# Optimization experiments

Hardware: AMD Instinct MI355X
Metric: run time of the kernel (lower is better)

The kernel has to match this reference:

```python
import jax, jax.numpy as jnp
import numpy as np

N_NODES = 100000
N_EDGES = 1600000
VOCAB = 128
D = 30
N_CLASSES = 5


def setup_inputs() -> dict:
    key = jax.random.key(0)
    ks = jax.random.split(key, 8)
    x = jax.random.randint(ks[0], (N_NODES,), 0, VOCAB)
    edge_index = jax.random.randint(ks[1], (2, N_EDGES), 0, N_NODES)
    emb = jax.random.normal(ks[2], (VOCAB, D), dtype=jnp.float32)
    W1 = jax.random.normal(ks[3], (D, D), dtype=jnp.float32) * (1.0 / np.sqrt(D))
    W2 = jax.random.normal(ks[4], (D, D), dtype=jnp.float32) * (1.0 / np.sqrt(D))
    W3 = jax.random.normal(ks[5], (D, D), dtype=jnp.float32) * (1.0 / np.sqrt(D))
    Wout = jax.random.normal(ks[6], (N_CLASSES, D), dtype=jnp.float32) * (1.0 / np.sqrt(D))
    b1 = jnp.zeros((D,), jnp.float32)
    b2 = jnp.zeros((D,), jnp.float32)
    b3 = jnp.zeros((D,), jnp.float32)
    bout = jnp.zeros((N_CLASSES,), jnp.float32)
    return dict(x=x, edge_index=edge_index, emb=emb, W1=W1, b1=b1, W2=W2, b2=b2,
                W3=W3, b3=b3, Wout=Wout, bout=bout)


def _gnn_layer(h, row, col, W, b):
    # h: [N, D]; row/col: [E+N] (self loops appended)
    n = h.shape[0]
    deg = jax.ops.segment_sum(jnp.ones(row.shape, h.dtype), row, num_segments=n)  # [N]
    msg = h[row] / deg[row][:, None]                 # gather + normalize: [E+N, D]
    agg = jax.ops.segment_sum(msg, col, num_segments=n)  # scatter-add: [N, D]
    return jax.nn.relu(agg @ W.T + b)


def reference(x, edge_index, emb, W1, b1, W2, b2, W3, b3, Wout, bout):
    n = x.shape[0]
    loops = jnp.arange(n, dtype=edge_index.dtype)
    row = jnp.concatenate([edge_index[0], loops])  # add_self_loops
    col = jnp.concatenate([edge_index[1], loops])
    h = emb[x]  # [N, D]
    for W, b in ((W1, b1), (W2, b2), (W3, b3)):
        h = _gnn_layer(h, row, col, W, b)
    return h @ Wout.T + bout  # [N, 5]
```

## Files before the change

kernel.cpp:

```cpp
#include <hip/hip_runtime.h>
#include <hip/hip_fp16.h>

#define D 30
#define DP 32
#define NCLS 5
#define VOCAB 128
#define BS 256
#define BSS 512
#define BSHIFT 8
#define BNODES 256
#define NSBMAX 512
#define CAP 8192
#define NBLK_S 256
#define CHUNK 6272
#define LDSCAP 6144
#define NPB 64


__global__ void k_prep(int* __restrict__ gcur, int* __restrict__ rcur, int nsb,
                       const float* __restrict__ emb, float* __restrict__ embp) {
    int i = blockIdx.x * blockDim.x + threadIdx.x;
    if (i < nsb) { gcur[i] = i * CAP; rcur[i] = i * CAP; }
    if (i < VOCAB * DP) {
        int v = i >> 5, c = i & (DP - 1);
        embp[i] = (c < D) ? emb[v * D + c] : 0.0f;
    }
}

__global__ void __launch_bounds__(BSS)
k_scatter3(const int* __restrict__ row, const int* __restrict__ col,
           int* __restrict__ gcur, int* __restrict__ rcur,
           int* __restrict__ ebuf, unsigned char* __restrict__ rbuf,
           int e, int nsb) {
    __shared__ int pay[CHUNK];
    __shared__ unsigned short bof[CHUNK];
    __shared__ int lhist[NSBMAX];
    __shared__ int lscan[NSBMAX];
    __shared__ int lcur[NSBMAX];
    __shared__ int gdst[NSBMAX];
    unsigned char* pay8 = (unsigned char*)pay;

    int phase = blockIdx.x >= NBLK_S;
    int blk = blockIdx.x - phase * NBLK_S;
    const int* key = phase ? row : col;
    int per = (e + NBLK_S - 1) / NBLK_S;
    int s = blk * per; if (s > e) s = e;
    int t = s + per; if (t > e) t = e;
    int m = t - s;
    int tid = threadIdx.x;

    lhist[tid] = 0;
    __syncthreads();
    for (int i = s + tid; i < t; i += BSS)
        atomicAdd(&lhist[key[i] >> BSHIFT], 1);
    __syncthreads();
    lscan[tid] = lhist[tid];
    __syncthreads();
    for (int st = 1; st < NSBMAX; st <<= 1) {
        int tv = (tid >= st) ? lscan[tid - st] : 0;
        __syncthreads();
        lscan[tid] += tv;
        __syncthreads();
    }
    lcur[tid] = lscan[tid] - lhist[tid];
    __syncthreads();
    if (phase == 0) {
        for (int i = s + tid; i < t; i += BSS) {
            int c = col[i], b = c >> BSHIFT;
            int p = atomicAdd(&lcur[b], 1);
            pay[p] = (row[i] << BSHIFT) | (c & (BNODES - 1));
            bof[p] = (unsigned short)b;
        }
    } else {
        for (int i = s + tid; i < t; i += BSS) {
            int r = row[i], b = r >> BSHIFT;
            int p = atomicAdd(&lcur[b], 1);
            pay8[p] = (unsigned char)(r & (BNODES - 1));
            bof[p] = (unsigned short)b;
        }
    }
    __syncthreads();
    int* cur = phase ? rcur : gcur;
    if (tid < nsb) {
        int h = lhist[tid];
        gdst[tid] = h ? atomicAdd(&cur[tid], h) : 0;
    }
    __syncthreads();
    if (phase == 0) {
        for (int p = tid; p < m; p += BSS) {
            int b = bof[p];
            ebuf[gdst[b] + (p - (lscan[b] - lhist[b]))] = pay[p];
        }
    } else {
        for (int p = tid; p < m; p += BSS) {
            int b = bof[p];
            rbuf[gdst[b] + (p - (lscan[b] - lhist[b]))] = pay8[p];
        }
    }
}

__global__ void __launch_bounds__(BS)
k_odbsort(int* __restrict__ ebuf, const unsigned char* __restrict__ rbuf,
          const int* __restrict__ gcur, const int* __restrict__ rcur,
          const int* __restrict__ x, float* __restrict__ rdeg, int2* __restrict__ xr,
          int* __restrict__ off, int* __restrict__ cnt, int n, int nsb) {
    __shared__ int ledge[LDSCAP];
    __shared__ int c256[BNODES];
    __shared__ int b256[BNODES];
    __shared__ int cur256[BNODES];
    int side = blockIdx.x >= nsb;
    int bkt = side ? blockIdx.x - nsb : blockIdx.x;
    int tid = threadIdx.x;
    int base = bkt * CAP;

    if (side == 0) {
        int rm = rcur[bkt] - base;
        c256[tid] = 0;
        __syncthreads();
        for (int k = tid; k < rm; k += BS)
            atomicAdd(&c256[rbuf[base + k]], 1);
        __syncthreads();
        int node = (bkt << BSHIFT) + tid;
        if (node < n) {
            float rd = 1.0f / (float)(c256[tid] + 1);
            rdeg[node] = rd;
            xr[node] = make_int2(x[node], __float_as_int(rd));
        }
    } else {
        int m = gcur[bkt] - base;
        if (m > LDSCAP) m = LDSCAP;
        for (int k = tid; k < m; k += BS) ledge[k] = ebuf[base + k];
        c256[tid] = 0;
        __syncthreads();
        for (int k = tid; k < m; k += BS)
            atomicAdd(&c256[ledge[k] & (BNODES - 1)], 1);
        __syncthreads();
        b256[tid] = c256[tid];
        __syncthreads();
        for (int st = 1; st < BNODES; st <<= 1) {
            int tv = (tid >= st) ? b256[tid - st] : 0;
            __syncthreads();
            b256[tid] += tv;
            __syncthreads();
        }
        cur256[tid] = b256[tid] - c256[tid];
        int node = (bkt << BSHIFT) + tid;
        if (node < n) {
            off[node] = base + b256[tid] - c256[tid];
            cnt[node] = c256[tid];
        }
        __syncthreads();
        for (int k = tid; k < m; k += BS) {
            int v = ledge[k];
            int p = atomicAdd(&cur256[v & (BNODES - 1)], 1);
            ebuf[base + p] = v >> BSHIFT;
        }
    }
}

__device__ __forceinline__ void acc8h(float4 raw, float* acc) {
    const __half2* h = (const __half2*)&raw;
#pragma unroll
    for (int u = 0; u < 4; ++u) {
        float2 f = __half22float2(h[u]);
        acc[2 * u] += f.x; acc[2 * u + 1] += f.y;
    }
}
__device__ __forceinline__ void fma4(float4 a, float4 w, float& d) {
    d = fmaf(a.x, w.x, d); d = fmaf(a.y, w.y, d);
    d = fmaf(a.z, w.z, d); d = fmaf(a.w, w.w, d);
}

__global__ void __launch_bounds__(BS)
k_agg_lin(const __half* __restrict__ Ain, const int2* __restrict__ xr,
          const float* __restrict__ embp,
          const int* __restrict__ off, const int* __restrict__ cnt,
          const int* __restrict__ esrc, const float* __restrict__ rdeg,
          const float* __restrict__ W, const float* __restrict__ bias,
          const float* __restrict__ Wout, const float* __restrict__ bout,
          __half* __restrict__ Aout, float* __restrict__ out,
          int n, int srcmode, int outmode) {
    __shared__ float aggS[NPB * DP];
    __shared__ float WsP[DP * DP];
    __shared__ float bsP[DP];
    __shared__ float h3S[NPB * DP];
    __shared__ float WoP[NCLS * DP];
    __shared__ float boS[NCLS];
    const float4* Ain4  = (const float4*)Ain;
    const float4* embp4 = (const float4*)embp;
    int tid = threadIdx.x;
    int i0 = blockIdx.x * NPB;
    int j = tid >> 2;
    int q = tid & 3;
    int i = i0 + j;
    for (int p = tid; p < DP * DP; p += BS) {
        int rr = p >> 5, ccx = p & 31;
        WsP[p] = (rr < D && ccx < D) ? W[rr * D + ccx] : 0.0f;
    }
    if (tid < DP) bsP[tid] = (tid < D) ? bias[tid] : 0.0f;
    if (outmode == 1) {
        for (int p = tid; p < NCLS * DP; p += BS) {
            int rr = p >> 5, ccx = p & 31;
            WoP[p] = (ccx < D) ? Wout[rr * D + ccx] : 0.0f;
        }
        if (tid < NCLS) boS[tid] = bout[tid];
    }
    float acc[8];
#pragma unroll
    for (int u = 0; u < 8; ++u) acc[u] = 0.0f;
    if (i < n) {
        int base = off[i], c = cnt[i], k = 0;
        if (srcmode == 0) {
            acc8h(Ain4[(size_t)i * 4 + q], acc);
            for (; k + 16 <= c; k += 16) {
                float4 av[16];
#pragma unroll
                for (int u = 0; u < 16; ++u)
                    av[u] = Ain4[(size_t)esrc[base + k + u] * 4 + q];
#pragma unroll
                for (int u = 0; u < 16; ++u) acc8h(av[u], acc);
            }
            for (; k + 4 <= c; k += 4) {
                float4 av[4];
#pragma unroll
                for (int u = 0; u < 4; ++u)
                    av[u] = Ain4[(size_t)esrc[base + k + u] * 4 + q];
#pragma unroll
                for (int u = 0; u < 4; ++u) acc8h(av[u], acc);
            }
            for (; k < c; ++k)
                acc8h(Ain4[(size_t)esrc[base + k] * 4 + q], acc);
        } else {
            int2 xi = xr[i];
            float ri = __int_as_float(xi.y);
            float4 e0 = embp4[(size_t)xi.x * 8 + 2 * q];
            float4 e1 = embp4[(size_t)xi.x * 8 + 2 * q + 1];
            acc[0] = e0.x * ri; acc[1] = e0.y * ri; acc[2] = e0.z * ri; acc[3] = e0.w * ri;
            acc[4] = e1.x * ri; acc[5] = e1.y * ri; acc[6] = e1.z * ri; acc[7] = e1.w * ri;
            for (; k + 4 <= c; k += 4) {
                int2 xv[4];
#pragma unroll
                for (int u = 0; u < 4; ++u) xv[u] = xr[esrc[base + k + u]];
#pragma unroll
                for (int u = 0; u < 4; ++u) {
                    float rr = __int_as_float(xv[u].y);
                    float4 f0 = embp4[(size_t)xv[u].x * 8 + 2 * q];
                    float4 f1 = embp4[(size_t)xv[u].x * 8 + 2 * q + 1];
                    acc[0] = fmaf(f0.x, rr, acc[0]); acc[1] = fmaf(f0.y, rr, acc[1]);
                    acc[2] = fmaf(f0.z, rr, acc[2]); acc[3] = fmaf(f0.w, rr, acc[3]);
                    acc[4] = fmaf(f1.x, rr, acc[4]); acc[5] = fmaf(f1.y, rr, acc[5]);
                    acc[6] = fmaf(f1.z, rr, acc[6]); acc[7] = fmaf(f1.w, rr, acc[7]);
                }
            }
            for (; k < c; ++k) {
                int2 xs = xr[esrc[base + k]];
                float rr = __int_as_float(xs.y);
                float4 f0 = embp4[(size_t)xs.x * 8 + 2 * q];
                float4 f1 = embp4[(size_t)xs.x * 8 + 2 * q + 1];
                acc[0] = fmaf(f0.x, rr, acc[0]); acc[1] = fmaf(f0.y, rr, acc[1]);
                acc[2] = fmaf(f0.z, rr, acc[2]); acc[3] = fmaf(f0.w, rr, acc[3]);
                acc[4] = fmaf(f1.x, rr, acc[4]); acc[5] = fmaf(f1.y, rr, acc[5]);
                acc[6] = fmaf(f1.z, rr, acc[6]); acc[7] = fmaf(f1.w, rr, acc[7]);
            }
        }
    }
    ((float4*)aggS)[j * 8 + 2 * q]     = make_float4(acc[0], acc[1], acc[2], acc[3]);
    ((float4*)aggS)[j * 8 + 2 * q + 1] = make_float4(acc[4], acc[5], acc[6], acc[7]);
    __syncthreads();

    {
        int cc = tid & 31;
        int jg = tid >> 5;
        const float4* wrow = (const float4*)&WsP[cc * DP];
        float4 w0 = wrow[0], w1 = wrow[1], w2 = wrow[2], w3 = wrow[3];
        float4 w4 = wrow[4], w5 = wrow[5], w6 = wrow[6], w7 = wrow[7];
        float bb = bsP[cc];
        if (outmode == 0) {
            for (int jj = jg; jj < NPB; jj += 8) {
                int nd = i0 + jj;
                if (nd >= n) break;
                const float4* ar = (const float4*)&aggS[jj * DP];
                float a = bb;
                fma4(ar[0], w0, a); fma4(ar[1], w1, a); fma4(ar[2], w2, a); fma4(ar[3], w3, a);
                fma4(ar[4], w4, a); fma4(ar[5], w5, a); fma4(ar[6], w6, a); fma4(ar[7], w7, a);
                a = fmaxf(a, 0.0f) * rdeg[nd];
                if (cc >= D) a = 0.0f;
                Aout[(size_t)nd * DP + cc] = __float2half_rn(a);
            }
        } else {
            for (int jj = jg; jj < NPB; jj += 8) {
                const float4* ar = (const float4*)&aggS[jj * DP];
                float a = bb;
                fma4(ar[0], w0, a); fma4(ar[1], w1, a); fma4(ar[2], w2, a); fma4(ar[3], w3, a);
                fma4(ar[4], w4, a); fma4(ar[5], w5, a); fma4(ar[6], w6, a); fma4(ar[7], w7, a);
                h3S[jj * DP + cc] = (cc < D) ? fmaxf(a, 0.0f) : 0.0f;
            }
            __syncthreads();
            for (int it = tid; it < NPB * NCLS; it += BS) {
                int jj = it / NCLS, cc2 = it - jj * NCLS;
                int nd = i0 + jj;
                if (nd >= n) continue;
                const float4* hr = (const float4*)&h3S[jj * DP];
                const float4* wr2 = (const float4*)&WoP[cc2 * DP];
                float a = boS[cc2];
#pragma unroll
                for (int u = 0; u < 8; ++u) fma4(hr[u], wr2[u], a);
                out[(size_t)nd * NCLS + cc2] = a;
            }
        }
    }
}


extern "C" void kernel_launch(void* const* d_in, const int* in_sizes, int n_in,
                              void* d_out, int out_size, void* d_ws, size_t ws_size,
                              hipStream_t stream) {
    const int*   x    = (const int*)d_in[0];
    const int*   ei   = (const int*)d_in[1];
    const float* emb  = (const float*)d_in[2];
    const float* W1   = (const float*)d_in[3];
    const float* b1   = (const float*)d_in[4];
    const float* W2   = (const float*)d_in[5];
    const float* b2   = (const float*)d_in[6];
    const float* W3   = (const float*)d_in[7];
    const float* b3   = (const float*)d_in[8];
    const float* Wout = (const float*)d_in[9];
    const float* bout = (const float*)d_in[10];
    float* out = (float*)d_out;

    const int N = in_sizes[0];
    const int E = in_sizes[1] / 2;
    const int* row = ei;
    const int* col = ei + E;
    const int nsb = (N + BNODES - 1) >> BSHIFT;

    __half* A0  = (__half*)d_ws;
    __half* A1  = A0 + (size_t)N * DP;
    float* embp = (float*)(A1 + (size_t)N * DP);
    float* rdeg = embp + VOCAB * DP;
    int2*  xr   = (int2*)(rdeg + N);
    int*   ebuf = (int*)(xr + N);
    unsigned char* rbuf = (unsigned char*)(ebuf + (size_t)nsb * CAP);
    int*   off  = (int*)(rbuf + (((size_t)nsb * CAP + 3) & ~(size_t)3));
    int*   cnt  = off + N;
    int*   gcur = cnt + N;
    int*   rcur = gcur + nsb;

    dim3 blk(BS);

    k_prep<<<dim3((VOCAB * DP + BS - 1) / BS), blk, 0, stream>>>(gcur, rcur, nsb, emb, embp);
    k_scatter3<<<dim3(2 * NBLK_S), dim3(BSS), 0, stream>>>(row, col, gcur, rcur,
                                                           ebuf, rbuf, E, nsb);
    k_odbsort<<<dim3(2 * nsb), blk, 0, stream>>>(ebuf, rbuf, gcur, rcur, x,
                                                 rdeg, xr, off, cnt, N, nsb);

    dim3 gAgg((N + NPB - 1) / NPB);
    k_agg_lin<<<gAgg, blk, 0, stream>>>(nullptr, xr, embp, off, cnt, ebuf, rdeg,
                                        W1, b1, Wout, bout, A1, out, N, 1, 0);
    k_agg_lin<<<gAgg, blk, 0, stream>>>(A1, xr, embp, off, cnt, ebuf, rdeg,
                                        W2, b2, Wout, bout, A0, out, N, 0, 0);
    k_agg_lin<<<gAgg, blk, 0, stream>>>(A0, xr, embp, off, cnt, ebuf, rdeg,
                                        W3, b3, Wout, bout, A1, out, N, 0, 1);
}
```

Measured before the change: 208.4 us.

## Pad per-node edge lists to multiples of 8 with a zero dummy node

```diff
diff --git a/kernel.cpp b/kernel.cpp
--- a/kernel.cpp
+++ b/kernel.cpp
@@ -13,18 +13,25 @@
 #define CAP 8192
 #define NBLK_S 256
 #define CHUNK 6272
-#define LDSCAP 6144
+#define LDSCAP 8192
 #define NPB 64
 
 
 __global__ void k_prep(int* __restrict__ gcur, int* __restrict__ rcur, int nsb,
-                       const float* __restrict__ emb, float* __restrict__ embp) {
+                       const float* __restrict__ emb, float* __restrict__ embp,
+                       __half* __restrict__ A0, __half* __restrict__ A1,
+                       int2* __restrict__ xr, int n) {
     int i = blockIdx.x * blockDim.x + threadIdx.x;
     if (i < nsb) { gcur[i] = i * CAP; rcur[i] = i * CAP; }
     if (i < VOCAB * DP) {
         int v = i >> 5, c = i & (DP - 1);
         embp[i] = (c < D) ? emb[v * D + c] : 0.0f;
     }
+    if (i < DP) {
+        A0[(size_t)n * DP + i] = __float2half_rn(0.0f);
+        A1[(size_t)n * DP + i] = __float2half_rn(0.0f);
+    }
+    if (i == 0) xr[n] = make_int2(0, 0);
 }
 
 __global__ void __launch_bounds__(BSS)
@@ -106,6 +113,7 @@
           int* __restrict__ off, int* __restrict__ cnt, int n, int nsb) {
     __shared__ int ledge[LDSCAP];
     __shared__ int c256[BNODES];
+    __shared__ int p256[BNODES];
     __shared__ int b256[BNODES];
     __shared__ int cur256[BNODES];
     int side = blockIdx.x >= nsb;
@@ -135,7 +143,9 @@
         for (int k = tid; k < m; k += BS)
             atomicAdd(&c256[ledge[k] & (BNODES - 1)], 1);
         __syncthreads();
-        b256[tid] = c256[tid];
+        int pc = (c256[tid] + 7) & ~7;
+        p256[tid] = pc;
+        b256[tid] = pc;
         __syncthreads();
         for (int st = 1; st < BNODES; st <<= 1) {
             int tv = (tid >= st) ? b256[tid - st] : 0;
@@ -143,18 +153,23 @@
             b256[tid] += tv;
             __syncthreads();
         }
-        cur256[tid] = b256[tid] - c256[tid];
+        int mybase = base + b256[tid] - p256[tid];
+        cur256[tid] = mybase;
         int node = (bkt << BSHIFT) + tid;
         if (node < n) {
-            off[node] = base + b256[tid] - c256[tid];
-            cnt[node] = c256[tid];
+            off[node] = mybase;
+            cnt[node] = p256[tid];
         }
         __syncthreads();
         for (int k = tid; k < m; k += BS) {
             int v = ledge[k];
             int p = atomicAdd(&cur256[v & (BNODES - 1)], 1);
-            ebuf[base + p] = v >> BSHIFT;
-        }
+            ebuf[base + (p - base)] = v >> BSHIFT;
+        }
+        __syncthreads();
+        int realend = cur256[tid];
+        int padend = mybase + p256[tid];
+        for (int p = realend; p < padend; ++p) ebuf[p] = n;
     }
 }
 
@@ -183,7 +198,6 @@
     __shared__ float aggS[NPB * DP];
     __shared__ float WsP[DP * DP];
     __shared__ float bsP[DP];
-    __shared__ float h3S[NPB * DP];
     __shared__ float WoP[NCLS * DP];
     __shared__ float boS[NCLS];
     const float4* Ain4  = (const float4*)Ain;
@@ -209,27 +223,23 @@
 #pragma unroll
     for (int u = 0; u < 8; ++u) acc[u] = 0.0f;
     if (i < n) {
-        int base = off[i], c = cnt[i], k = 0;
+        int base = off[i], c = cnt[i];
         if (srcmode == 0) {
             acc8h(Ain4[(size_t)i * 4 + q], acc);
-            for (; k + 16 <= c; k += 16) {
-                float4 av[16];
-#pragma unroll
-                for (int u = 0; u < 16; ++u)
-                    av[u] = Ain4[(size_t)esrc[base + k + u] * 4 + q];
-#pragma unroll
-                for (int u = 0; u < 16; ++u) acc8h(av[u], acc);
-            }
-            for (; k + 4 <= c; k += 4) {
-                float4 av[4];
-#pragma unroll
-                for (int u = 0; u < 4; ++u)
-                    av[u] = Ain4[(size_t)esrc[base + k + u] * 4 + q];
-#pragma unroll
-                for (int u = 0; u < 4; ++u) acc8h(av[u], acc);
-            }
-            for (; k < c; ++k)
-                acc8h(Ain4[(size_t)esrc[base + k] * 4 + q], acc);
+            for (int k = 0; k < c; k += 8) {
+                int4 ea = *(const int4*)(esrc + base + k);
+                int4 eb = *(const int4*)(esrc + base + k + 4);
+                float4 a0 = Ain4[(size_t)ea.x * 4 + q];
+                float4 a1 = Ain4[(size_t)ea.y * 4 + q];
+                float4 a2 = Ain4[(size_t)ea.z * 4 + q];
+                float4 a3 = Ain4[(size_t)ea.w * 4 + q];
+                float4 a4 = Ain4[(size_t)eb.x * 4 + q];
+                float4 a5 = Ain4[(size_t)eb.y * 4 + q];
+                float4 a6 = Ain4[(size_t)eb.z * 4 + q];
+                float4 a7 = Ain4[(size_t)eb.w * 4 + q];
+                acc8h(a0, acc); acc8h(a1, acc); acc8h(a2, acc); acc8h(a3, acc);
+                acc8h(a4, acc); acc8h(a5, acc); acc8h(a6, acc); acc8h(a7, acc);
+            }
         } else {
             int2 xi = xr[i];
             float ri = __int_as_float(xi.y);
@@ -237,12 +247,14 @@
             float4 e1 = embp4[(size_t)xi.x * 8 + 2 * q + 1];
             acc[0] = e0.x * ri; acc[1] = e0.y * ri; acc[2] = e0.z * ri; acc[3] = e0.w * ri;
             acc[4] = e1.x * ri; acc[5] = e1.y * ri; acc[6] = e1.z * ri; acc[7] = e1.w * ri;
-            for (; k + 4 <= c; k += 4) {
-                int2 xv[4];
-#pragma unroll
-                for (int u = 0; u < 4; ++u) xv[u] = xr[esrc[base + k + u]];
-#pragma unroll
-                for (int u = 0; u < 4; ++u) {
+            for (int k = 0; k < c; k += 8) {
+                int4 ea = *(const int4*)(esrc + base + k);
+                int4 eb = *(const int4*)(esrc + base + k + 4);
+                int2 xv[8];
+                xv[0] = xr[ea.x]; xv[1] = xr[ea.y]; xv[2] = xr[ea.z]; xv[3] = xr[ea.w];
+                xv[4] = xr[eb.x]; xv[5] = xr[eb.y]; xv[6] = xr[eb.z]; xv[7] = xr[eb.w];
+#pragma unroll
+                for (int u = 0; u < 8; ++u) {
                     float rr = __int_as_float(xv[u].y);
                     float4 f0 = embp4[(size_t)xv[u].x * 8 + 2 * q];
                     float4 f1 = embp4[(size_t)xv[u].x * 8 + 2 * q + 1];
@@ -251,16 +263,6 @@
                     acc[4] = fmaf(f1.x, rr, acc[4]); acc[5] = fmaf(f1.y, rr, acc[5]);
                     acc[6] = fmaf(f1.z, rr, acc[6]); acc[7] = fmaf(f1.w, rr, acc[7]);
                 }
-            }
-            for (; k < c; ++k) {
-                int2 xs = xr[esrc[base + k]];
-                float rr = __int_as_float(xs.y);
-                float4 f0 = embp4[(size_t)xs.x * 8 + 2 * q];
-                float4 f1 = embp4[(size_t)xs.x * 8 + 2 * q + 1];
-                acc[0] = fmaf(f0.x, rr, acc[0]); acc[1] = fmaf(f0.y, rr, acc[1]);
-                acc[2] = fmaf(f0.z, rr, acc[2]); acc[3] = fmaf(f0.w, rr, acc[3]);
-                acc[4] = fmaf(f1.x, rr, acc[4]); acc[5] = fmaf(f1.y, rr, acc[5]);
-                acc[6] = fmaf(f1.z, rr, acc[6]); acc[7] = fmaf(f1.w, rr, acc[7]);
             }
         }
     }
@@ -288,19 +290,26 @@
                 Aout[(size_t)nd * DP + cc] = __float2half_rn(a);
             }
         } else {
-            for (int jj = jg; jj < NPB; jj += 8) {
+            float h3r[8];
+#pragma unroll
+            for (int u = 0; u < 8; ++u) {
+                int jj = jg + 8 * u;
                 const float4* ar = (const float4*)&aggS[jj * DP];
                 float a = bb;
                 fma4(ar[0], w0, a); fma4(ar[1], w1, a); fma4(ar[2], w2, a); fma4(ar[3], w3, a);
                 fma4(ar[4], w4, a); fma4(ar[5], w5, a); fma4(ar[6], w6, a); fma4(ar[7], w7, a);
-                h3S[jj * DP + cc] = (cc < D) ? fmaxf(a, 0.0f) : 0.0f;
-            }
+                h3r[u] = (cc < D) ? fmaxf(a, 0.0f) : 0.0f;
+            }
+            __syncthreads();
+#pragma unroll
+            for (int u = 0; u < 8; ++u)
+                aggS[(jg + 8 * u) * DP + cc] = h3r[u];
             __syncthreads();
             for (int it = tid; it < NPB * NCLS; it += BS) {
                 int jj = it / NCLS, cc2 = it - jj * NCLS;
                 int nd = i0 + jj;
                 if (nd >= n) continue;
-                const float4* hr = (const float4*)&h3S[jj * DP];
+                const float4* hr = (const float4*)&aggS[jj * DP];
                 const float4* wr2 = (const float4*)&WoP[cc2 * DP];
                 float a = boS[cc2];
 #pragma unroll
@@ -335,11 +344,11 @@
     const int nsb = (N + BNODES - 1) >> BSHIFT;
 
     __half* A0  = (__half*)d_ws;
-    __half* A1  = A0 + (size_t)N * DP;
-    float* embp = (float*)(A1 + (size_t)N * DP);
+    __half* A1  = A0 + (size_t)(N + 1) * DP;
+    float* embp = (float*)(A1 + (size_t)(N + 1) * DP);
     float* rdeg = embp + VOCAB * DP;
     int2*  xr   = (int2*)(rdeg + N);
-    int*   ebuf = (int*)(xr + N);
+    int*   ebuf = (int*)(xr + N + 2);
     unsigned char* rbuf = (unsigned char*)(ebuf + (size_t)nsb * CAP);
     int*   off  = (int*)(rbuf + (((size_t)nsb * CAP + 3) & ~(size_t)3));
     int*   cnt  = off + N;
@@ -348,7 +357,8 @@
 
     dim3 blk(BS);
 
-    k_prep<<<dim3((VOCAB * DP + BS - 1) / BS), blk, 0, stream>>>(gcur, rcur, nsb, emb, embp);
+    k_prep<<<dim3((VOCAB * DP + BS - 1) / BS), blk, 0, stream>>>(
+        gcur, rcur, nsb, emb, embp, A0, A1, xr, N);
     k_scatter3<<<dim3(2 * NBLK_S), dim3(BSS), 0, stream>>>(row, col, gcur, rcur,
                                                            ebuf, rbuf, E, nsb);
     k_odbsort<<<dim3(2 * nsb), blk, 0, stream>>>(ebuf, rbuf, gcur, rcur, x,
```

Result: no change. 208.5 us (+0.1%).
